# Kernel optimization log

Hardware: AMD Instinct MI355X
Metric: run time of the kernel (lower is better)

## Reference

```python
import jax, jax.numpy as jnp
import numpy as np

C, K, DIL = 128, 3, 1
PAD = DIL
KK = K * K
EPS = 1e-5


def setup_inputs() -> dict:
    key = jax.random.key(0)
    k0, k1, k2 = jax.random.split(key, 3)
    B, H, W = 8, 128, 128
    x = jax.random.normal(k0, (B, C, H, W), jnp.float32)
    # small offset-conv weights so predicted offsets are realistic (sub-pixel scale)
    w_off = jax.random.normal(k1, (2 * KK, C, K, K), jnp.float32) * 0.01
    b_off = jnp.zeros((2 * KK,), jnp.float32)
    w_dw = jax.random.normal(k2, (C, 1, K, K), jnp.float32) * (1.0 / 3.0)
    gamma = jnp.ones((C,), jnp.float32)
    beta = jnp.zeros((C,), jnp.float32)
    return {"x": x, "w_off": w_off, "b_off": b_off, "w_dw": w_dw,
            "gamma": gamma, "beta": beta}


def _deform_depthwise(x, offset, w_dw):
    """torchvision-style deform_conv2d, groups=C (depthwise), stride=1."""
    B, C_, H, W = x.shape
    off = offset.reshape(B, KK, 2, H, W)  # (y,x) pairs per kernel tap
    hs = jnp.arange(H, dtype=x.dtype)[None, None, :, None]
    ws = jnp.arange(W, dtype=x.dtype)[None, None, None, :]
    ki = jnp.arange(K, dtype=x.dtype)
    ky = jnp.repeat(ki, K)  # [KK] row index of tap
    kx = jnp.tile(ki, K)    # [KK] col index of tap
    # sampling positions: base grid + dilated tap offset - pad + learned offset
    py = hs + (DIL * ky - PAD)[None, :, None, None] + off[:, :, 0]  # [B,KK,H,W]
    px = ws + (DIL * kx - PAD)[None, :, None, None] + off[:, :, 1]
    y0 = jnp.floor(py)
    x0 = jnp.floor(px)
    ty = py - y0
    tx = px - x0
    y0i = y0.astype(jnp.int32)
    x0i = x0.astype(jnp.int32)

    def gather(xb, yi, xi):
        # zero outside the image (torchvision zero-pad semantics)
        valid = (yi >= 0) & (yi < H) & (xi >= 0) & (xi < W)
        yc = jnp.clip(yi, 0, H - 1)
        xc = jnp.clip(xi, 0, W - 1)
        v = xb[:, yc, xc]  # [C,KK,H,W]
        return v * valid[None].astype(xb.dtype)

    def sample_one(xb, y0b, x0b, tyb, txb):
        v00 = gather(xb, y0b, x0b)
        v01 = gather(xb, y0b, x0b + 1)
        v10 = gather(xb, y0b + 1, x0b)
        v11 = gather(xb, y0b + 1, x0b + 1)
        w00 = (1 - tyb) * (1 - txb)
        w01 = (1 - tyb) * txb
        w10 = tyb * (1 - txb)
        w11 = tyb * txb
        return (v00 * w00[None] + v01 * w01[None]
                + v10 * w10[None] + v11 * w11[None])  # [C,KK,H,W]

    val = jax.vmap(sample_one)(x, y0i, x0i, ty, tx)  # [B,C,KK,H,W]
    # depthwise contraction over the KK taps
    return jnp.einsum('bckhw,ck->bchw', val, w_dw.reshape(C, KK))


def reference(x, w_off, b_off, w_dw, gamma, beta):
    identity = x
    offset = jax.lax.conv_general_dilated(
        x, w_off, window_strides=(1, 1), padding=[(PAD, PAD), (PAD, PAD)],
        dimension_numbers=('NCHW', 'OIHW', 'NCHW'))
    offset = offset + b_off[None, :, None, None]
    out = _deform_depthwise(x, offset, w_dw)
    # BatchNorm2d in training mode (batch statistics), then SiLU
    mean = jnp.mean(out, axis=(0, 2, 3), keepdims=True)
    var = jnp.mean((out - mean) ** 2, axis=(0, 2, 3), keepdims=True)
    out = (out - mean) * jax.lax.rsqrt(var + EPS)
    out = out * gamma[None, :, None, None] + beta[None, :, None, None]
    out = out * jax.nn.sigmoid(out)  # SiLU
    return out + identity
```

## Files before the change

kernel.cpp:

```cpp
#include <hip/hip_runtime.h>
#include <hip/hip_fp16.h>
#include <math.h>

#define Cc 128
#define Hh 128
#define Ww 128
#define Bb 8
#define HW 16384
#define NPIX 131072
#define NOFF 18

typedef unsigned int u32;
typedef _Float16 half8 __attribute__((ext_vector_type(8)));
typedef __attribute__((ext_vector_type(16))) float f32x16;

static __device__ __forceinline__ u32 pack2h(float a, float b){
  __half2 h = __floats2half2_rn(a, b);
  return *(u32*)&h;
}

__global__ __launch_bounds__(256) void k_repack(const float* __restrict__ w_off, const float* __restrict__ w_dw,
                                                u32* __restrict__ wBf, u32* __restrict__ wdt_h){
  int i = blockIdx.x*256 + threadIdx.x;
  if (i < 72*64*4){
    int step = i >> 8;
    int r    = i & 255;
    int lane = r >> 2;
    int q    = r & 3;
    int tap  = step / 8, chunk = step % 8;
    int o    = lane & 31, half = lane >> 5;
    int c0   = chunk*16 + half*8 + 2*q;
    float v0 = (o < NOFF) ? w_off[(size_t)(o*Cc + c0    )*9 + tap] : 0.f;
    float v1 = (o < NOFF) ? w_off[(size_t)(o*Cc + c0 + 1)*9 + tap] : 0.f;
    wBf[i] = pack2h(v0, v1);
  }
  int j = i - 72*64*4;
  if (j >= 0 && j < 9*64){
    int cp = j & 63; int k = j >> 6;
    wdt_h[j] = pack2h(w_dw[(2*cp)*9 + k], w_dw[(2*cp+1)*9 + k]);
  }
}

__global__ __launch_bounds__(256) void k_tx(const float* __restrict__ x, u32* __restrict__ xt16){
  __shared__ float t[128][65];
  int tid = threadIdx.x;
  int b   = blockIdx.x >> 8;
  int hw0 = (blockIdx.x & 255) << 6;
  int lane = tid & 63, wg = tid >> 6;
  const float* xb = x + (size_t)b*Cc*HW;
  #pragma unroll
  for (int k=0;k<32;k++){
    int c = wg + k*4;
    t[c][lane] = xb[(size_t)c*HW + hw0 + lane];
  }
  __syncthreads();
  u32* ob = xt16 + ((size_t)b*HW + hw0)*64;
  int cpair = tid & 63, grp = tid >> 6;
  #pragma unroll
  for (int k=0;k<16;k++){
    int hwl = grp + k*4;
    ob[(size_t)hwl*64 + cpair] = pack2h(t[cpair*2][hwl], t[cpair*2+1][hwl]);
  }
}

__global__ __launch_bounds__(256) void k_offset_mfma(const u32* __restrict__ xt, const u32* __restrict__ wBf,
                                                     const float* __restrict__ b_off, u32* __restrict__ recs){
  __shared__ float piv[128][21];
  int tid = threadIdx.x, lane = tid & 63, wid = tid >> 6;
  int b = blockIdx.x >> 7, h = blockIdx.x & 127;
  int row = lane & 31, half = lane >> 5;
  int w0 = wid*32;
  int w = w0 + row;

  const u32* xb = xt + (size_t)b*HW*64;

  int taddr[9]; bool tval[9];
  #pragma unroll
  for (int t=0;t<9;t++){
    int ky = t/3 - 1, kx = t%3 - 1;
    int hh = h + ky, wt = w + kx;
    bool v = (hh>=0)&&(hh<Hh)&&(wt>=0)&&(wt<Ww);
    int hwd = hh*Ww + wt;
    hwd = min(max(hwd,0),HW-1);
    taddr[t] = hwd*64 + half*4;
    tval[t] = v;
  }

  f32x16 acc;
  #pragma unroll
  for (int i=0;i<16;i++) acc[i] = 0.f;

  const uint4* wb = (const uint4*)wBf;
  #pragma unroll 1
  for (int t=0;t<9;t++){
    const uint4* ap = (const uint4*)(xb + taddr[t]);
    bool v = tval[t];
    #pragma unroll
    for (int ch=0;ch<8;ch++){
      uint4 a = ap[ch*2];
      if (!v){ a.x=0u; a.y=0u; a.z=0u; a.w=0u; }
      uint4 bf = wb[(t*8+ch)*64 + lane];
      acc = __builtin_amdgcn_mfma_f32_32x32x16_f16(*(half8*)&a, *(half8*)&bf, acc, 0, 0, 0);
    }
  }

  int o = lane & 31;
  #pragma unroll
  for (int r=0;r<16;r++){
    int pxl = w0 + ((r&3) + 8*(r>>2) + 4*half);
    if (o < NOFF) piv[pxl][o] = acc[r];
  }
  __syncthreads();

  if (tid < 128){
    int wpx = tid;
    float v[NOFF];
    #pragma unroll
    for (int oo=0;oo<NOFF;oo++) v[oo] = piv[wpx][oo] + b_off[oo];

    u32 rec[36];
    #pragma unroll
    for (int kk=0;kk<9;kk++){
      float py = (float)(h + kk/3 - 1) + v[2*kk];
      float qx = (float)(wpx + kk%3 - 1) + v[2*kk+1];
      float fy = floorf(py), fx = floorf(qx);
      float ty = py - fy, tx = qx - fx;
      int y0 = (int)fy, x0 = (int)fx;
      int y1 = y0+1, x1 = x0+1;
      bool vy0 = (y0>=0)&&(y0<Hh), vy1=(y1>=0)&&(y1<Hh);
      bool vx0 = (x0>=0)&&(x0<Ww), vx1=(x1>=0)&&(x1<Ww);
      u32 yc0 = (u32)(min(max(y0,0),Hh-1)*Ww), yc1 = (u32)(min(max(y1,0),Hh-1)*Ww);
      u32 xc0 = (u32)min(max(x0,0),Ww-1),      xc1 = (u32)min(max(x1,0),Ww-1);
      rec[2*kk]   = (yc0+xc0) | ((yc0+xc1)<<16);
      rec[2*kk+1] = (yc1+xc0) | ((yc1+xc1)<<16);
      float c00 = (vy0&&vx0) ? (1.f-ty)*(1.f-tx) : 0.f;
      float c01 = (vy0&&vx1) ? (1.f-ty)*tx       : 0.f;
      float c10 = (vy1&&vx0) ? ty*(1.f-tx)       : 0.f;
      float c11 = (vy1&&vx1) ? ty*tx             : 0.f;
      rec[18+2*kk] = pack2h(c00, c01);
      rec[19+2*kk] = pack2h(c10, c11);
    }
    int pxg = blockIdx.x*128 + wpx;
    uint4* dst = (uint4*)(recs + (size_t)pxg*36);
    #pragma unroll
    for (int q=0;q<9;q++) dst[q] = *(uint4*)(rec + q*4);
  }
}

template<bool F16OUT>
__global__ __launch_bounds__(256) void k_deform_rec(const u32* __restrict__ xt, const u32* __restrict__ recs,
                                                    const u32* __restrict__ wdt_h, float* __restrict__ out,
                                                    u32* __restrict__ dwb, float* __restrict__ bps){
  __shared__ float pivot[16][132];
  int tid = threadIdx.x, lane = tid & 63, wid = tid >> 6;
  int pxb = blockIdx.x * 16;
  int bu = pxb >> 14, hw0 = pxb & 16383;
  int l2 = lane*2;

  __half2 wk2[9];
  #pragma unroll
  for (int k=0;k<9;k++){
    u32 wv = wdt_h[k*64 + lane];
    wk2[k] = *(__half2*)&wv;
  }

  const u32* xbu = xt + (size_t)bu*HW*64;

  #pragma unroll
  for (int i=0;i<4;i++){
    int pu = __builtin_amdgcn_readfirstlane(pxb + wid*4 + i);
    const u32* rec = recs + (size_t)pu*36;

    u32 q[9][4];
    #pragma unroll
    for (int kk=0;kk<9;kk++){
      u32 dA = rec[2*kk], dB = rec[2*kk+1];
      q[kk][0] = xbu[(size_t)(dA & 0xFFFFu)*64 + lane];
      q[kk][1] = xbu[(size_t)(dA >> 16)   *64 + lane];
      q[kk][2] = xbu[(size_t)(dB & 0xFFFFu)*64 + lane];
      q[kk][3] = xbu[(size_t)(dB >> 16)   *64 + lane];
    }

    __half2 acc2 = __floats2half2_rn(0.f, 0.f);
    #pragma unroll
    for (int kk=0;kk<9;kk++){
      u32 uA = rec[18+2*kk], uB = rec[19+2*kk];
      __half2 hA = *(__half2*)&uA, hB = *(__half2*)&uB;
      __half2 q0 = *(__half2*)&q[kk][0], q1 = *(__half2*)&q[kk][1];
      __half2 q2 = *(__half2*)&q[kk][2], q3 = *(__half2*)&q[kk][3];
      __half2 s = __hmul2(__low2half2(hA), q0);
      s = __hfma2(__high2half2(hA), q1, s);
      s = __hfma2(__low2half2(hB),  q2, s);
      s = __hfma2(__high2half2(hB), q3, s);
      acc2 = __hfma2(wk2[kk], s, acc2);
    }
    pivot[wid*4+i][l2]   = __low2float(acc2);
    pivot[wid*4+i][l2+1] = __high2float(acc2);
  }
  __syncthreads();
  #pragma unroll
  for (int it=0; it<2; it++){
    int c = (tid>>2) + it*64, qd = tid & 3;
    float4 r = make_float4(pivot[qd*4+0][c], pivot[qd*4+1][c], pivot[qd*4+2][c], pivot[qd*4+3][c]);
    float s  = (r.x + r.y) + (r.z + r.w);
    float s2 = fmaf(r.x,r.x, fmaf(r.y,r.y, fmaf(r.z,r.z, r.w*r.w)));
    s  += __shfl_down(s, 2, 4);  s  += __shfl_down(s, 1, 4);
    s2 += __shfl_down(s2, 2, 4); s2 += __shfl_down(s2, 1, 4);
    if (qd == 0){
      bps[(size_t)blockIdx.x*256 + c]       = s;
      bps[(size_t)blockIdx.x*256 + 128 + c] = s2;
    }
    if (F16OUT){
      uint2 pp; pp.x = pack2h(r.x, r.y); pp.y = pack2h(r.z, r.w);
      *(uint2*)&dwb[(((size_t)bu*Cc + c)*HW + hw0)/2 + qd*2] = pp;
    } else {
      *(float4*)(out + ((size_t)bu*Cc + c)*HW + hw0 + qd*4) = r;
    }
  }
}

__global__ __launch_bounds__(256) void k_statsr1(const float* __restrict__ bps, float* __restrict__ part2){
  int tid = threadIdx.x;
  size_t base = (size_t)blockIdx.x * 64;
  float a = 0.f;
  for (int r=0;r<64;r++) a += bps[(base + r)*256 + tid];
  part2[blockIdx.x*256 + tid] = a;
}

__global__ __launch_bounds__(256) void k_statsr2(const float* __restrict__ part2, float* __restrict__ mr){
  __shared__ float t[256];
  int tid = threadIdx.x;
  float a = 0.f;
  for (int r=0;r<128;r++) a += part2[r*256 + tid];
  t[tid] = a;
  __syncthreads();
  if (tid < 128){
    float S = t[tid], S2 = t[128 + tid];
    const float invN = 1.f/(float)(Bb*HW);
    float m = S*invN;
    float var = S2*invN - m*m;
    mr[tid]       = m;
    mr[Cc + tid]  = rsqrtf(var + 1e-5f);
  }
}

__global__ __launch_bounds__(256) void k_apply_f32(float* __restrict__ out, const float* __restrict__ x,
                                                   const float* __restrict__ mr, const float* __restrict__ gamma,
                                                   const float* __restrict__ beta){
  int i = blockIdx.x*256 + threadIdx.x;
  int c = (i >> 12) & 127;
  float4 v  = ((const float4*)out)[i];
  float4 xi = ((const float4*)x)[i];
  float m = mr[c], r = mr[Cc+c], g = gamma[c], be = beta[c];
  float* vp = (float*)&v; const float* xp = (const float*)&xi;
  float4 o; float* op = (float*)&o;
  #pragma unroll
  for (int j=0;j<4;j++){
    float t = (vp[j]-m)*r*g + be;
    t = t / (1.f + expf(-t));
    op[j] = t + xp[j];
  }
  ((float4*)out)[i] = o;
}

__global__ __launch_bounds__(256) void k_apply_f16(const u32* __restrict__ dwb, float* __restrict__ out,
                                                   const float* __restrict__ x, const float* __restrict__ mr,
                                                   const float* __restrict__ gamma, const float* __restrict__ beta){
  int i = blockIdx.x*256 + threadIdx.x;
  int c = (i >> 12) & 127;
  uint2 dw = ((const uint2*)dwb)[i];
  float4 xi = ((const float4*)x)[i];
  float m = mr[c], r = mr[Cc+c], g = gamma[c], be = beta[c];
  __half2 d0 = *(__half2*)&dw.x, d1 = *(__half2*)&dw.y;
  float v[4];
  v[0] = __low2float(d0); v[1] = __high2float(d0);
  v[2] = __low2float(d1); v[3] = __high2float(d1);
  const float* xp = (const float*)&xi;
  float4 o; float* op = (float*)&o;
  #pragma unroll
  for (int j=0;j<4;j++){
    float t = (v[j]-m)*r*g + be;
    t = t / (1.f + expf(-t));
    op[j] = t + xp[j];
  }
  ((float4*)out)[i] = o;
}

extern "C" void kernel_launch(void* const* d_in, const int* in_sizes, int n_in,
                              void* d_out, int out_size, void* d_ws, size_t ws_size,
                              hipStream_t stream) {
  const float* x     = (const float*)d_in[0];
  const float* w_off = (const float*)d_in[1];
  const float* b_off = (const float*)d_in[2];
  const float* w_dw  = (const float*)d_in[3];
  const float* gamma = (const float*)d_in[4];
  const float* beta  = (const float*)d_in[5];
  float* out = (float*)d_out;

  u32*   wBf  = (u32*)d_ws;
  u32*   wdt_h= (u32*)d_ws + 23040;
  float* mr   = (float*)d_ws + 24576;
  u32*   recs = (u32*)d_ws + 32768;
  u32*   xt16 = recs + (size_t)NPIX*36;
  float* bps  = (float*)(xt16 + (size_t)NPIX*64);
  float* part2= bps + (size_t)8192*256;
  u32*   dwb  = (u32*)(part2 + 128*256);

  const size_t NEED_B = ((size_t)32768 + (size_t)NPIX*36 + (size_t)NPIX*64
                         + (size_t)8192*256 + 128*256 + (size_t)NPIX*64) * 4;
  bool big = (ws_size >= NEED_B);

  hipLaunchKernelGGL(k_repack, dim3((72*64*4 + 9*64 + 255)/256), dim3(256), 0, stream, w_off, w_dw, wBf, wdt_h);
  hipLaunchKernelGGL(k_tx,     dim3(2048), dim3(256), 0, stream, x, xt16);
  hipLaunchKernelGGL(k_offset_mfma, dim3(1024), dim3(256), 0, stream, xt16, wBf, b_off, recs);

  if (big){
    hipLaunchKernelGGL((k_deform_rec<true>), dim3(NPIX/16), dim3(256), 0, stream, xt16, recs, wdt_h, out, dwb, bps);
  } else {
    hipLaunchKernelGGL((k_deform_rec<false>), dim3(NPIX/16), dim3(256), 0, stream, xt16, recs, wdt_h, out, dwb, bps);
  }
  hipLaunchKernelGGL(k_statsr1, dim3(128), dim3(256), 0, stream, bps, part2);
  hipLaunchKernelGGL(k_statsr2, dim3(1),   dim3(256), 0, stream, part2, mr);
  if (big){
    hipLaunchKernelGGL(k_apply_f16, dim3(NPIX*Cc/4/256), dim3(256), 0, stream, dwb, out, x, mr, gamma, beta);
  } else {
    hipLaunchKernelGGL(k_apply_f32, dim3(NPIX*Cc/4/256), dim3(256), 0, stream, out, x, mr, gamma, beta);
  }
}
```

Before: 158.1 us.

## Stage 3-row input halo tile in LDS for offset conv MFMA

```diff
diff --git a/kernel.cpp b/kernel.cpp
--- a/kernel.cpp
+++ b/kernel.cpp
@@ -63,60 +63,74 @@
   }
 }
 
-__global__ __launch_bounds__(256) void k_offset_mfma(const u32* __restrict__ xt, const u32* __restrict__ wBf,
+__global__ __launch_bounds__(128) void k_offset_mfma(const u32* __restrict__ xt, const u32* __restrict__ wBf,
                                                      const float* __restrict__ b_off, u32* __restrict__ recs){
-  __shared__ float piv[128][21];
-  int tid = threadIdx.x, lane = tid & 63, wid = tid >> 6;
-  int b = blockIdx.x >> 7, h = blockIdx.x & 127;
+  __shared__ u32 xl[3][68][65];
+  float* pivf = (float*)&xl[0][0][0];
+  int tid = threadIdx.x, lane = tid & 63, wv = tid >> 6;
+  int b  = blockIdx.x >> 8;
+  int rm = blockIdx.x & 255;
+  int h  = rm >> 1, wh = rm & 1;
   int row = lane & 31, half = lane >> 5;
-  int w0 = wid*32;
-  int w = w0 + row;
+  int w = wh*64 + wv*32 + row;
+  int w0c = wh*64 - 2;
 
   const u32* xb = xt + (size_t)b*HW*64;
 
-  int taddr[9]; bool tval[9];
+  for (int i = tid; i < 3*68*16; i += 128){
+    int q = i & 15; int t2 = i >> 4; int p = t2 % 68; int r = t2 / 68;
+    int hh = min(max(h + r - 1, 0), Hh-1);
+    int gc = min(max(w0c + p, 0), Ww-1);
+    *(uint4*)&xl[r][p][q*4] = *(const uint4*)(xb + ((size_t)(hh*Ww + gc))*64 + q*4);
+  }
+  __syncthreads();
+
+  bool tval[9]; int tpd[9];
   #pragma unroll
   for (int t=0;t<9;t++){
-    int ky = t/3 - 1, kx = t%3 - 1;
-    int hh = h + ky, wt = w + kx;
-    bool v = (hh>=0)&&(hh<Hh)&&(wt>=0)&&(wt<Ww);
-    int hwd = hh*Ww + wt;
-    hwd = min(max(hwd,0),HW-1);
-    taddr[t] = hwd*64 + half*4;
-    tval[t] = v;
-  }
-
-  f32x16 acc;
-  #pragma unroll
-  for (int i=0;i<16;i++) acc[i] = 0.f;
-
+    int ky = t/3 - 1, dx = t%3 - 1;
+    int hh = h + ky, wt = w + dx;
+    tval[t] = (hh>=0)&&(hh<Hh)&&(wt>=0)&&(wt<Ww);
+    int p = wv*32 + row + 2 + dx;
+    tpd[t] = (t/3)*4420 + p*65 + half*4;
+  }
+
+  f32x16 accE, accO;
+  #pragma unroll
+  for (int i=0;i<16;i++){ accE[i]=0.f; accO[i]=0.f; }
+
+  const u32* xl0 = &xl[0][0][0];
   const uint4* wb = (const uint4*)wBf;
   #pragma unroll 1
   for (int t=0;t<9;t++){
-    const uint4* ap = (const uint4*)(xb + taddr[t]);
     bool v = tval[t];
+    int base = tpd[t];
     #pragma unroll
     for (int ch=0;ch<8;ch++){
-      uint4 a = ap[ch*2];
+      uint4 a = *(const uint4*)(xl0 + base + ch*8);
       if (!v){ a.x=0u; a.y=0u; a.z=0u; a.w=0u; }
       uint4 bf = wb[(t*8+ch)*64 + lane];
-      acc = __builtin_amdgcn_mfma_f32_32x32x16_f16(*(half8*)&a, *(half8*)&bf, acc, 0, 0, 0);
-    }
-  }
+      if (ch & 1) accO = __builtin_amdgcn_mfma_f32_32x32x16_f16(*(half8*)&a, *(half8*)&bf, accO, 0, 0, 0);
+      else        accE = __builtin_amdgcn_mfma_f32_32x32x16_f16(*(half8*)&a, *(half8*)&bf, accE, 0, 0, 0);
+    }
+  }
+  f32x16 acc = accE + accO;
+
+  __syncthreads();
 
   int o = lane & 31;
   #pragma unroll
   for (int r=0;r<16;r++){
-    int pxl = w0 + ((r&3) + 8*(r>>2) + 4*half);
-    if (o < NOFF) piv[pxl][o] = acc[r];
-  }
-  __syncthreads();
-
-  if (tid < 128){
-    int wpx = tid;
+    int pxl = wv*32 + ((r&3) + 8*(r>>2) + 4*half);
+    if (o < NOFF) pivf[pxl*21 + o] = acc[r];
+  }
+  __syncthreads();
+
+  if (tid < 64){
+    int wpx = wh*64 + tid;
     float v[NOFF];
     #pragma unroll
-    for (int oo=0;oo<NOFF;oo++) v[oo] = piv[wpx][oo] + b_off[oo];
+    for (int oo=0;oo<NOFF;oo++) v[oo] = pivf[tid*21 + oo] + b_off[oo];
 
     u32 rec[36];
     #pragma unroll
@@ -140,7 +154,7 @@
       rec[18+2*kk] = pack2h(c00, c01);
       rec[19+2*kk] = pack2h(c10, c11);
     }
-    int pxg = blockIdx.x*128 + wpx;
+    int pxg = b*HW + h*Ww + wpx;
     uint4* dst = (uint4*)(recs + (size_t)pxg*36);
     #pragma unroll
     for (int q=0;q<9;q++) dst[q] = *(uint4*)(rec + q*4);
@@ -312,7 +326,7 @@
 
   hipLaunchKernelGGL(k_repack, dim3((72*64*4 + 9*64 + 255)/256), dim3(256), 0, stream, w_off, w_dw, wBf, wdt_h);
   hipLaunchKernelGGL(k_tx,     dim3(2048), dim3(256), 0, stream, x, xt16);
-  hipLaunchKernelGGL(k_offset_mfma, dim3(1024), dim3(256), 0, stream, xt16, wBf, b_off, recs);
+  hipLaunchKernelGGL(k_offset_mfma, dim3(2048), dim3(128), 0, stream, xt16, wBf, b_off, recs);
 
   if (big){
     hipLaunchKernelGGL((k_deform_rec<true>), dim3(NPIX/16), dim3(256), 0, stream, xt16, recs, wdt_h, out, dwb, bps);
```

Measured after the change: 173.3 us. 1.1x slower.
